# Kernel tuning notes

Measured on AMD Instinct MI355X. Metric: run time of the kernel, lower is better.

The kernel has to match this reference:

```python
import jax, jax.numpy as jnp
import numpy as np

T = 8          # number of adapter tasks
H = 1024       # hidden_size
I = 4096       # intermediate_size (bert dense input)
D = H // 16    # adapter bottleneck (reduction_factor=16)
B, S = 8, 512
EPS = 1e-12    # BERT LayerNorm eps


def _layernorm(x, g, b):
    mu = jnp.mean(x, axis=-1, keepdims=True)
    var = jnp.mean(jnp.square(x - mu), axis=-1, keepdims=True)
    return (x - mu) * jax.lax.rsqrt(var + EPS) * g + b


def setup_inputs() -> dict:
    key = jax.random.key(0)
    ks = jax.random.split(key, 14)
    std = 0.02
    inp = {
        "hidden_states": jax.random.normal(ks[0], (B, S, I), jnp.float32),
        "input_tensor": jax.random.normal(ks[1], (B, S, H), jnp.float32),
        "dense_w": jax.random.normal(ks[2], (H, I), jnp.float32) * std,
        "dense_b": jnp.zeros((H,), jnp.float32),
        "ln_g": jnp.ones((H,), jnp.float32),
        "ln_b": jnp.zeros((H,), jnp.float32),
        "down_w": jax.random.normal(ks[3], (T, D, H), jnp.float32) * std,
        "down_b": jnp.zeros((T, D), jnp.float32),
        "up_w": jax.random.normal(ks[4], (T, H, D), jnp.float32) * std,
        "up_b": jnp.zeros((T, H), jnp.float32),
        "key_w": jax.random.normal(ks[5], (H, H), jnp.float32) * std,
        "key_b": jnp.zeros((H,), jnp.float32),
        "query_w": jax.random.normal(ks[6], (H, H), jnp.float32) * std,
        "query_b": jnp.zeros((H,), jnp.float32),
        # value init: near-zero with identity diagonal
        "value_w": jnp.full((H, H), 1e-6, jnp.float32).at[jnp.arange(H), jnp.arange(H)].set(1.0),
    }
    return inp


def reference(hidden_states, input_tensor, dense_w, dense_b, ln_g, ln_b,
              down_w, down_b, up_w, up_b, key_w, key_b, query_w, query_b, value_w):
    # dense: [B,S,I] @ [H,I]^T -> [B,S,H]   (dropout = identity in eval)
    h = jnp.einsum('bsi,hi->bsh', hidden_states, dense_w) + dense_b
    prenorm = input_tensor + h
    adapter_in = _layernorm(prenorm, ln_g, ln_b)
    # batched per-task adapters: down-project, relu, up-project -> [T,B,S,H]
    down = jax.nn.relu(jnp.einsum('bsh,tdh->tbsd', adapter_in, down_w)
                       + down_b[:, None, None, :])
    adapter_out = jnp.einsum('tbsd,thd->tbsh', down, up_w) + up_b[:, None, None, :]
    # fusion attention over task axis T
    key = jnp.einsum('tbsh,kh->tbsk', adapter_out, key_w) + key_b
    value = jnp.einsum('tbsh,vh->tbsv', adapter_out + h[None], value_w)
    query = jnp.einsum('bsh,qh->bsq', prenorm, query_w) + query_b
    scores = jnp.sum(query[None] * key, axis=-1, keepdims=True)  # [T,B,S,1]
    probs = jax.nn.softmax(scores, axis=0)
    fusion = jnp.sum(probs * value, axis=0)                       # [B,S,H]
    return _layernorm(input_tensor + fusion, ln_g, ln_b)
```

## Files before the change

### kernel.cpp

```cpp
#include <hip/hip_runtime.h>
#include <cstdint>
#include <cstddef>

typedef float   f32x4 __attribute__((ext_vector_type(4)));
typedef _Float16 f16x8 __attribute__((ext_vector_type(8)));
typedef _Float16 f16x4 __attribute__((ext_vector_type(4)));

#define TOK  4096
#define HID  1024
#define IDIM 4096
#define LDP  40

__global__ __launch_bounds__(256, 4) void gemm_sk(
    const float* __restrict__ Af, const _Float16* __restrict__ B,
    int K, int Kchunk, float* __restrict__ part)
{
    __shared__ _Float16 lA[128 * LDP];
    __shared__ _Float16 lB[128 * LDP];
    const int tid  = threadIdx.x;
    const int lane = tid & 63;
    const int wave = tid >> 6;
    const int m0   = blockIdx.x * 128;
    const int n0   = blockIdx.y * 128;
    const int kz0  = blockIdx.z * Kchunk;
    const int wM   = (wave & 1) * 64;
    const int wN   = (wave >> 1) * 64;

    f32x4 acc[4][4] = {};

    for (int k0 = kz0; k0 < kz0 + Kchunk; k0 += 32) {
#pragma unroll
        for (int j = 0; j < 2; ++j) {
            const int q   = tid + j * 256;
            const int row = q >> 2;
            const int kc  = q & 3;
            const float* src = Af + (size_t)(m0 + row) * K + k0 + kc * 8;
            f32x4 v0 = *(const f32x4*)src;
            f32x4 v1 = *(const f32x4*)(src + 4);
            f16x8 o;
            o[0] = (_Float16)v0[0]; o[1] = (_Float16)v0[1];
            o[2] = (_Float16)v0[2]; o[3] = (_Float16)v0[3];
            o[4] = (_Float16)v1[0]; o[5] = (_Float16)v1[1];
            o[6] = (_Float16)v1[2]; o[7] = (_Float16)v1[3];
            *(f16x8*)(lA + row * LDP + kc * 8) = o;
            uint4 vb = *(const uint4*)(B + (size_t)(n0 + row) * K + k0 + kc * 8);
            *(uint4*)(lB + row * LDP + kc * 8) = vb;
        }
        __syncthreads();
        const int fr  = lane & 15;
        const int kc8 = (lane >> 4) * 8;
        f16x8 afr[4], bfr[4];
#pragma unroll
        for (int mi = 0; mi < 4; ++mi)
            afr[mi] = *(const f16x8*)(lA + (wM + mi * 16 + fr) * LDP + kc8);
#pragma unroll
        for (int ni = 0; ni < 4; ++ni)
            bfr[ni] = *(const f16x8*)(lB + (wN + ni * 16 + fr) * LDP + kc8);
#pragma unroll
        for (int mi = 0; mi < 4; ++mi)
#pragma unroll
            for (int ni = 0; ni < 4; ++ni)
                acc[mi][ni] = __builtin_amdgcn_mfma_f32_16x16x32_f16(
                    afr[mi], bfr[ni], acc[mi][ni], 0, 0, 0);
        __syncthreads();
    }

    float* dst = part + (size_t)blockIdx.z * TOK * HID;
    const int cn = lane & 15;
    const int rq = (lane >> 4) * 4;
#pragma unroll
    for (int mi = 0; mi < 4; ++mi)
#pragma unroll
        for (int r = 0; r < 4; ++r) {
            const int m = m0 + wM + mi * 16 + rq + r;
#pragma unroll
            for (int ni = 0; ni < 4; ++ni) {
                const int n = n0 + wN + ni * 16 + cn;
                dst[(size_t)m * HID + n] = acc[mi][ni][r];
            }
        }
}

template <int MODE>
__global__ __launch_bounds__(1024, 4) void gemm_w32(
    const _Float16* __restrict__ Ah, const _Float16* __restrict__ B,
    int K, int Ncols,
    float* __restrict__ outF, _Float16* __restrict__ outH,
    const float* __restrict__ bias, const float* __restrict__ addv,
    const float* __restrict__ probs, const float* __restrict__ upb,
    const _Float16* __restrict__ A2, const _Float16* __restrict__ B2,
    _Float16* __restrict__ outH2)
{
    __shared__ _Float16 lA[128 * LDP];
    __shared__ _Float16 lB[128 * LDP];
    const int tid  = threadIdx.x;
    const int lane = tid & 63;
    const int wave = tid >> 6;
    const int m0   = blockIdx.x * 128;
    int n0, half = 0;
    const _Float16* Ap = Ah;
    const _Float16* Bp = B;
    if constexpr (MODE == 5) {
        half = blockIdx.y >> 2;
        n0 = (blockIdx.y & 3) * 128;
        if (half) { Ap = A2; Bp = B2; }
    } else {
        n0 = blockIdx.y * 128;
    }
    const int wM = (wave & 3) * 32;
    const int wN = (wave >> 2) * 32;

    f32x4 acc[2][2] = {};

    const int st   = tid & 511;
    const int srow = st >> 2;
    const int sc   = (st & 3) * 8;
    const _Float16* sbase = (tid < 512)
        ? Ap + (size_t)(m0 + srow) * K + sc
        : Bp + (size_t)(n0 + srow) * K + sc;
    _Float16* sdst = ((tid < 512) ? lA : lB) + srow * LDP + sc;

    for (int k0 = 0; k0 < K; k0 += 32) {
        *(uint4*)sdst = *(const uint4*)(sbase + k0);
        __syncthreads();
        const int fr  = lane & 15;
        const int kc8 = (lane >> 4) * 8;
        f16x8 afr[2], bfr[2];
#pragma unroll
        for (int mi = 0; mi < 2; ++mi)
            afr[mi] = *(const f16x8*)(lA + (wM + mi * 16 + fr) * LDP + kc8);
#pragma unroll
        for (int ni = 0; ni < 2; ++ni)
            bfr[ni] = *(const f16x8*)(lB + (wN + ni * 16 + fr) * LDP + kc8);
#pragma unroll
        for (int mi = 0; mi < 2; ++mi)
#pragma unroll
            for (int ni = 0; ni < 2; ++ni)
                acc[mi][ni] = __builtin_amdgcn_mfma_f32_16x16x32_f16(
                    afr[mi], bfr[ni], acc[mi][ni], 0, 0, 0);
        __syncthreads();
    }

    const int cn = lane & 15;
    const int rq = (lane >> 4) * 4;
#pragma unroll
    for (int mi = 0; mi < 2; ++mi)
#pragma unroll
        for (int r = 0; r < 4; ++r) {
            const int m = m0 + wM + mi * 16 + rq + r;
#pragma unroll
            for (int ni = 0; ni < 2; ++ni) {
                const int n = n0 + wN + ni * 16 + cn;
                const float v = acc[mi][ni][r];
                if constexpr (MODE == 1) {
                    const float bb = bias ? bias[n] : 0.f;
                    outH[(size_t)m * Ncols + n] = (_Float16)(v + bb);
                } else if constexpr (MODE == 3) {
                    const size_t idx = (size_t)m * Ncols + n;
                    float s = v + addv[idx];
#pragma unroll
                    for (int t = 0; t < 8; ++t)
                        s += probs[(size_t)m * 8 + t] * upb[t * 1024 + n];
                    outH[idx] = (_Float16)s;
                } else if constexpr (MODE == 4) {
                    const size_t idx = (size_t)m * Ncols + n;
                    outF[idx] = v + addv[idx];
                } else {
                    const size_t idx = (size_t)m * 512 + n;
                    if (half == 0) {
                        const float y = v + bias[n];
                        outH[idx] = (_Float16)(y > 0.f ? y : 0.f);
                    } else {
                        outH2[idx] = (_Float16)v;
                    }
                }
            }
        }
}

__global__ __launch_bounds__(256) void ln_fused(
    const float* __restrict__ part, int sk,
    const float* __restrict__ dbias, const float* __restrict__ it,
    const float* __restrict__ gam, const float* __restrict__ bet,
    float* __restrict__ h_f32, _Float16* __restrict__ ai, _Float16* __restrict__ pn)
{
    const int n = blockIdx.x, tid = threadIdx.x;
    const int lane = tid & 63, wave = tid >> 6;
    const size_t base = (size_t)n * 1024 + tid * 4;
    f32x4 h = *(const f32x4*)(dbias + tid * 4);
    for (int z = 0; z < sk; ++z)
        h += *(const f32x4*)(part + (size_t)z * TOK * HID + base);
    *(f32x4*)(h_f32 + base) = h;
    f32x4 x = h + *(const f32x4*)(it + base);
    float s = x[0] + x[1] + x[2] + x[3];
    float q = x[0] * x[0] + x[1] * x[1] + x[2] * x[2] + x[3] * x[3];
#pragma unroll
    for (int off = 1; off < 64; off <<= 1) {
        s += __shfl_xor(s, off);
        q += __shfl_xor(q, off);
    }
    __shared__ float rs[4], rq[4];
    if (lane == 0) { rs[wave] = s; rq[wave] = q; }
    __syncthreads();
    s = rs[0] + rs[1] + rs[2] + rs[3];
    q = rq[0] + rq[1] + rq[2] + rq[3];
    const float mu = s * (1.f / 1024.f);
    const float var = q * (1.f / 1024.f) - mu * mu;
    const float rstd = rsqrtf(var + 1e-12f);
    f32x4 gv = *(const f32x4*)(gam + tid * 4);
    f32x4 bv = *(const f32x4*)(bet + tid * 4);
    f16x4 av, pv;
#pragma unroll
    for (int j = 0; j < 4; ++j) {
        const float y = (x[j] - mu) * rstd * gv[j] + bv[j];
        av[j] = (_Float16)y;
        pv[j] = (_Float16)x[j];
    }
    *(f16x4*)(ai + base) = av;
    *(f16x4*)(pn + base) = pv;
}

__global__ __launch_bounds__(256) void ln_out(
    const float* __restrict__ fuse, const float* __restrict__ gam,
    const float* __restrict__ bet, float* __restrict__ outp)
{
    const int n = blockIdx.x, tid = threadIdx.x;
    const int lane = tid & 63, wave = tid >> 6;
    const size_t base = (size_t)n * 1024 + tid * 4;
    f32x4 x = *(const f32x4*)(fuse + base);
    float s = x[0] + x[1] + x[2] + x[3];
    float q = x[0] * x[0] + x[1] * x[1] + x[2] * x[2] + x[3] * x[3];
#pragma unroll
    for (int off = 1; off < 64; off <<= 1) {
        s += __shfl_xor(s, off);
        q += __shfl_xor(q, off);
    }
    __shared__ float rs[4], rq[4];
    if (lane == 0) { rs[wave] = s; rq[wave] = q; }
    __syncthreads();
    s = rs[0] + rs[1] + rs[2] + rs[3];
    q = rq[0] + rq[1] + rq[2] + rq[3];
    const float mu = s * (1.f / 1024.f);
    const float var = q * (1.f / 1024.f) - mu * mu;
    const float rstd = rsqrtf(var + 1e-12f);
    f32x4 gv = *(const f32x4*)(gam + tid * 4);
    f32x4 bv = *(const f32x4*)(bet + tid * 4);
    f32x4 y;
#pragma unroll
    for (int j = 0; j < 4; ++j) y[j] = (x[j] - mu) * rstd * gv[j] + bv[j];
    *(f32x4*)(outp + base) = y;
}

__global__ __launch_bounds__(256) void scores_softmax(
    const _Float16* __restrict__ qk, const _Float16* __restrict__ query,
    const float* __restrict__ key_b, const float* __restrict__ up_b,
    const _Float16* __restrict__ down, const _Float16* __restrict__ g,
    float* __restrict__ probs_out, _Float16* __restrict__ wdown)
{
    const int n = blockIdx.x, tid = threadIdx.x;
    const int lane = tid & 63, wave = tid >> 6;
    const _Float16* qkrow = qk + (size_t)n * 1024;
    const _Float16* qrow  = query + (size_t)n * 1024;
    float ub[8] = {};
    float qb = 0.f;
#pragma unroll
    for (int j = 0; j < 4; ++j) {
        const int h = tid + j * 256;
        const float qkv = (float)qkrow[h];
        qb += (float)qrow[h] * key_b[h];
#pragma unroll
        for (int t = 0; t < 8; ++t) ub[t] += qkv * up_b[t * 1024 + h];
    }
#pragma unroll
    for (int off = 1; off < 64; off <<= 1) {
        qb += __shfl_xor(qb, off);
#pragma unroll
        for (int t = 0; t < 8; ++t) ub[t] += __shfl_xor(ub[t], off);
    }
    __shared__ float red[4][9];
    __shared__ float sd[8];
    __shared__ float pl[8];
    if (lane == 0) {
        red[wave][0] = qb;
#pragma unroll
        for (int t = 0; t < 8; ++t) red[wave][1 + t] = ub[t];
    }
    const int c0 = tid * 2;
    const size_t dbase = (size_t)n * 512;
    const float d0 = (float)down[dbase + c0];
    const float d1 = (float)down[dbase + c0 + 1];
    float pz = d0 * (float)g[dbase + c0] + d1 * (float)g[dbase + c0 + 1];
#pragma unroll
    for (int off = 1; off < 32; off <<= 1) pz += __shfl_xor(pz, off);
    if ((lane & 31) == 0) sd[wave * 2 + (lane >> 5)] = pz;
    __syncthreads();
    if (tid == 0) {
        const float qbt = red[0][0] + red[1][0] + red[2][0] + red[3][0];
        float sc[8];
        float mx = -1e30f;
#pragma unroll
        for (int t = 0; t < 8; ++t) {
            sc[t] = sd[t] + qbt + red[0][1 + t] + red[1][1 + t] + red[2][1 + t] + red[3][1 + t];
            mx = fmaxf(mx, sc[t]);
        }
        float sum = 0.f;
#pragma unroll
        for (int t = 0; t < 8; ++t) { sc[t] = expf(sc[t] - mx); sum += sc[t]; }
        const float inv = 1.f / sum;
#pragma unroll
        for (int t = 0; t < 8; ++t) pl[t] = sc[t] * inv;
    }
    __syncthreads();
    const float pr = pl[c0 >> 6];
    wdown[dbase + c0]     = (_Float16)(pr * d0);
    wdown[dbase + c0 + 1] = (_Float16)(pr * d1);
    if (tid < 8) probs_out[(size_t)n * 8 + tid] = pl[tid];
}

__device__ inline void cvt_seg(const float* __restrict__ s, _Float16* __restrict__ d,
                               int n4, int gid, int gsz)
{
    for (int i = gid; i < n4; i += gsz) {
        f32x4 v = ((const f32x4*)s)[i];
        f16x4 o;
        o[0] = (_Float16)v[0]; o[1] = (_Float16)v[1];
        o[2] = (_Float16)v[2]; o[3] = (_Float16)v[3];
        ((f16x4*)d)[i] = o;
    }
}

__global__ __launch_bounds__(256) void convert4(
    const float* s0, _Float16* d0, int n0,
    const float* s1, _Float16* d1, int n1,
    const float* s2, _Float16* d2, int n2,
    const float* s3, _Float16* d3, int n3)
{
    const int gid = blockIdx.x * 256 + threadIdx.x;
    const int gsz = gridDim.x * 256;
    cvt_seg(s0, d0, n0, gid, gsz);
    cvt_seg(s1, d1, n1, gid, gsz);
    cvt_seg(s2, d2, n2, gid, gsz);
    cvt_seg(s3, d3, n3, gid, gsz);
}

__global__ __launch_bounds__(256) void transpose_kw(
    const float* __restrict__ in, _Float16* __restrict__ outp)
{
    __shared__ float t[32][33];
    const int bx = blockIdx.x * 32;
    const int by = blockIdx.y * 32;
    const int tx = threadIdx.x & 31, ty = threadIdx.x >> 5;
#pragma unroll
    for (int j = 0; j < 32; j += 8)
        t[ty + j][tx] = in[(size_t)(by + ty + j) * 1024 + bx + tx];
    __syncthreads();
#pragma unroll
    for (int j = 0; j < 32; j += 8)
        outp[(size_t)(bx + ty + j) * 1024 + by + tx] = (_Float16)t[tx][ty + j];
}

__global__ __launch_bounds__(256) void reshape_up(
    const float* __restrict__ up_w, _Float16* __restrict__ upg,
    _Float16* __restrict__ upmix)
{
    const int i = blockIdx.x * 256 + threadIdx.x;
    const int d = i & 63;
    const int h = (i >> 6) & 1023;
    const int t = i >> 16;
    const float v = up_w[i];
    upg[(size_t)(t * 64 + d) * 1024 + h] = (_Float16)v;
    upmix[(size_t)h * 512 + t * 64 + d]  = (_Float16)v;
}

extern "C" void kernel_launch(void* const* d_in, const int* in_sizes, int n_in,
                              void* d_out, int out_size, void* d_ws, size_t ws_size,
                              hipStream_t stream)
{
    const float* hs      = (const float*)d_in[0];
    const float* it      = (const float*)d_in[1];
    const float* dense_w = (const float*)d_in[2];
    const float* dense_b = (const float*)d_in[3];
    const float* ln_g    = (const float*)d_in[4];
    const float* ln_b    = (const float*)d_in[5];
    const float* down_w  = (const float*)d_in[6];
    const float* down_b  = (const float*)d_in[7];
    const float* up_w    = (const float*)d_in[8];
    const float* up_b    = (const float*)d_in[9];
    const float* key_w   = (const float*)d_in[10];
    const float* key_b   = (const float*)d_in[11];
    const float* query_w = (const float*)d_in[12];
    const float* query_b = (const float*)d_in[13];
    const float* value_w = (const float*)d_in[14];
    float* outp = (float*)d_out;
    (void)in_sizes; (void)n_in; (void)out_size;

    const size_t MiB = 1ull << 20;
    char* p = (char*)d_ws;
    _Float16* w_dense = (_Float16*)p;  p += 8 * MiB;
    _Float16* w_query = (_Float16*)p;  p += 2 * MiB;
    _Float16* w_keyT  = (_Float16*)p;  p += 2 * MiB;
    _Float16* w_value = (_Float16*)p;  p += 2 * MiB;
    _Float16* w_down  = (_Float16*)p;  p += 1 * MiB;
    _Float16* w_upg   = (_Float16*)p;  p += 1 * MiB;
    _Float16* w_upmix = (_Float16*)p;  p += 1 * MiB;
    float*    h_f32   = (float*)p;     p += 16 * MiB;
    _Float16* ai      = (_Float16*)p;  p += 8 * MiB;
    _Float16* pn      = (_Float16*)p;  p += 8 * MiB;
    char* rb = p;
    const int sk = (ws_size >= (size_t)(49 + 64) * MiB) ? 4 : 2;
    float*    part  = (float*)rb;
    _Float16* query = (_Float16*)rb;
    _Float16* qk    = (_Float16*)(rb +  8 * MiB);
    _Float16* down  = (_Float16*)(rb + 16 * MiB);
    _Float16* g     = (_Float16*)(rb + 20 * MiB);
    _Float16* wdown = (_Float16*)(rb + 24 * MiB);
    float*    probs = (float*)(rb + 28 * MiB);
    float*    fuse  = (float*)rb;
    _Float16* mixed = ai;

    convert4<<<1024, 256, 0, stream>>>(dense_w, w_dense, HID * IDIM / 4,
                                       query_w, w_query, HID * HID / 4,
                                       value_w, w_value, HID * HID / 4,
                                       down_w,  w_down,  512 * HID / 4);
    transpose_kw<<<dim3(32, 32), 256, 0, stream>>>(key_w, w_keyT);
    reshape_up<<<2048, 256, 0, stream>>>(up_w, w_upg, w_upmix);

    gemm_sk<<<dim3(32, 8, sk), 256, 0, stream>>>(hs, w_dense, IDIM, IDIM / sk, part);
    ln_fused<<<TOK, 256, 0, stream>>>(part, sk, dense_b, it, ln_g, ln_b, h_f32, ai, pn);
    gemm_w32<1><<<dim3(32, 8), 1024, 0, stream>>>(
        pn, w_query, HID, HID, nullptr, query, query_b, nullptr, nullptr, nullptr,
        nullptr, nullptr, nullptr);
    gemm_w32<1><<<dim3(32, 8), 1024, 0, stream>>>(
        query, w_keyT, HID, HID, nullptr, qk, nullptr, nullptr, nullptr, nullptr,
        nullptr, nullptr, nullptr);
    gemm_w32<5><<<dim3(32, 8), 1024, 0, stream>>>(
        ai, w_down, HID, 512, nullptr, down, down_b, nullptr, nullptr, nullptr,
        qk, w_upg, g);
    scores_softmax<<<TOK, 256, 0, stream>>>(qk, query, key_b, up_b, down, g, probs, wdown);
    gemm_w32<3><<<dim3(32, 8), 1024, 0, stream>>>(
        wdown, w_upmix, 512, HID, nullptr, mixed, nullptr, h_f32, probs, up_b,
        nullptr, nullptr, nullptr);
    gemm_w32<4><<<dim3(32, 8), 1024, 0, stream>>>(
        mixed, w_value, HID, HID, fuse, nullptr, nullptr, it, nullptr, nullptr,
        nullptr, nullptr, nullptr);
    ln_out<<<TOK, 256, 0, stream>>>(fuse, ln_g, ln_b, outp);
}
```

Before: 400.8 us.

## Pre-convert hidden_states to fp16 and load dense GEMM tiles via global_load_lds

```diff
diff --git a/kernel.cpp b/kernel.cpp
--- a/kernel.cpp
+++ b/kernel.cpp
@@ -11,12 +11,16 @@
 #define IDIM 4096
 #define LDP  40
 
-__global__ __launch_bounds__(256, 4) void gemm_sk(
-    const float* __restrict__ Af, const _Float16* __restrict__ B,
+#define GLDS16(gp, lp) __builtin_amdgcn_global_load_lds(                      \
+    (const __attribute__((address_space(1))) void*)(gp),                      \
+    (__attribute__((address_space(3))) void*)(lp), 16, 0, 0)
+
+__global__ __launch_bounds__(256, 2) void gemm_dense(
+    const _Float16* __restrict__ A, const _Float16* __restrict__ B,
     int K, int Kchunk, float* __restrict__ part)
 {
-    __shared__ _Float16 lA[128 * LDP];
-    __shared__ _Float16 lB[128 * LDP];
+    __shared__ _Float16 lA[128 * 32];
+    __shared__ _Float16 lB[128 * 32];
     const int tid  = threadIdx.x;
     const int lane = tid & 63;
     const int wave = tid >> 6;
@@ -26,36 +30,30 @@
     const int wM   = (wave & 1) * 64;
     const int wN   = (wave >> 1) * 64;
 
+    const int srow = wave * 32 + (lane >> 2);
+    const int scol = (lane & 3) * 8;
+    const _Float16* gA = A + (size_t)(m0 + srow) * K + kz0 + scol;
+    const _Float16* gB = B + (size_t)(n0 + srow) * K + kz0 + scol;
+    _Float16* sA = lA + wave * 1024;
+    _Float16* sB = lB + wave * 1024;
+
     f32x4 acc[4][4] = {};
-
-    for (int k0 = kz0; k0 < kz0 + Kchunk; k0 += 32) {
-#pragma unroll
-        for (int j = 0; j < 2; ++j) {
-            const int q   = tid + j * 256;
-            const int row = q >> 2;
-            const int kc  = q & 3;
-            const float* src = Af + (size_t)(m0 + row) * K + k0 + kc * 8;
-            f32x4 v0 = *(const f32x4*)src;
-            f32x4 v1 = *(const f32x4*)(src + 4);
-            f16x8 o;
-            o[0] = (_Float16)v0[0]; o[1] = (_Float16)v0[1];
-            o[2] = (_Float16)v0[2]; o[3] = (_Float16)v0[3];
-            o[4] = (_Float16)v1[0]; o[5] = (_Float16)v1[1];
-            o[6] = (_Float16)v1[2]; o[7] = (_Float16)v1[3];
-            *(f16x8*)(lA + row * LDP + kc * 8) = o;
-            uint4 vb = *(const uint4*)(B + (size_t)(n0 + row) * K + k0 + kc * 8);
-            *(uint4*)(lB + row * LDP + kc * 8) = vb;
-        }
+    const int fr  = lane & 15;
+    const int kc8 = (lane >> 4) * 8;
+
+    for (int k = 0; k < Kchunk; k += 32) {
+        GLDS16(gA + k,          sA);
+        GLDS16(gA + k + 16 * K, sA + 512);
+        GLDS16(gB + k,          sB);
+        GLDS16(gB + k + 16 * K, sB + 512);
         __syncthreads();
-        const int fr  = lane & 15;
-        const int kc8 = (lane >> 4) * 8;
         f16x8 afr[4], bfr[4];
 #pragma unroll
         for (int mi = 0; mi < 4; ++mi)
-            afr[mi] = *(const f16x8*)(lA + (wM + mi * 16 + fr) * LDP + kc8);
+            afr[mi] = *(const f16x8*)(lA + (wM + mi * 16 + fr) * 32 + kc8);
 #pragma unroll
         for (int ni = 0; ni < 4; ++ni)
-            bfr[ni] = *(const f16x8*)(lB + (wN + ni * 16 + fr) * LDP + kc8);
+            bfr[ni] = *(const f16x8*)(lB + (wN + ni * 16 + fr) * 32 + kc8);
 #pragma unroll
         for (int mi = 0; mi < 4; ++mi)
 #pragma unroll
@@ -329,11 +327,12 @@
     }
 }
 
-__global__ __launch_bounds__(256) void convert4(
+__global__ __launch_bounds__(256) void convert5(
     const float* s0, _Float16* d0, int n0,
     const float* s1, _Float16* d1, int n1,
     const float* s2, _Float16* d2, int n2,
-    const float* s3, _Float16* d3, int n3)
+    const float* s3, _Float16* d3, int n3,
+    const float* s4, _Float16* d4, int n4)
 {
     const int gid = blockIdx.x * 256 + threadIdx.x;
     const int gsz = gridDim.x * 256;
@@ -341,6 +340,7 @@
     cvt_seg(s1, d1, n1, gid, gsz);
     cvt_seg(s2, d2, n2, gid, gsz);
     cvt_seg(s3, d3, n3, gid, gsz);
+    cvt_seg(s4, d4, n4, gid, gsz);
 }
 
 __global__ __launch_bounds__(256) void transpose_kw(
@@ -407,8 +407,9 @@
     _Float16* ai      = (_Float16*)p;  p += 8 * MiB;
     _Float16* pn      = (_Float16*)p;  p += 8 * MiB;
     char* rb = p;
-    const int sk = (ws_size >= (size_t)(49 + 64) * MiB) ? 4 : 2;
+    const int sk = 2;
     float*    part  = (float*)rb;
+    _Float16* hs_h  = (_Float16*)(rb + 32 * MiB);
     _Float16* query = (_Float16*)rb;
     _Float16* qk    = (_Float16*)(rb +  8 * MiB);
     _Float16* down  = (_Float16*)(rb + 16 * MiB);
@@ -417,15 +418,17 @@
     float*    probs = (float*)(rb + 28 * MiB);
     float*    fuse  = (float*)rb;
     _Float16* mixed = ai;
-
-    convert4<<<1024, 256, 0, stream>>>(dense_w, w_dense, HID * IDIM / 4,
+    (void)ws_size;
+
+    convert5<<<2048, 256, 0, stream>>>(hs, hs_h, TOK * IDIM / 4,
+                                       dense_w, w_dense, HID * IDIM / 4,
                                        query_w, w_query, HID * HID / 4,
                                        value_w, w_value, HID * HID / 4,
                                        down_w,  w_down,  512 * HID / 4);
     transpose_kw<<<dim3(32, 32), 256, 0, stream>>>(key_w, w_keyT);
     reshape_up<<<2048, 256, 0, stream>>>(up_w, w_upg, w_upmix);
 
-    gemm_sk<<<dim3(32, 8, sk), 256, 0, stream>>>(hs, w_dense, IDIM, IDIM / sk, part);
+    gemm_dense<<<dim3(32, 8, sk), 256, 0, stream>>>(hs_h, w_dense, IDIM, IDIM / sk, part);
     ln_fused<<<TOK, 256, 0, stream>>>(part, sk, dense_b, it, ln_g, ln_b, h_f32, ai, pn);
     gemm_w32<1><<<dim3(32, 8), 1024, 0, stream>>>(
         pn, w_query, HID, HID, nullptr, query, query_b, nullptr, nullptr, nullptr,
```

Result: faster. 384.6 us (-4.0%).
